# Kernel optimization log

Measured on AMD Instinct MI355X. Metric: run time of the kernel, lower is better.

The kernel has to match this reference:

```python
import jax, jax.numpy as jnp
import numpy as np

N_NODES = 100000
N_EDGES = 1600000
D_FEAT = 64
HIDDEN = 64


def _glorot(key, shape):
    fan_in, fan_out = shape[1], shape[0]
    limit = float(np.sqrt(6.0 / (fan_in + fan_out)))
    return jax.random.uniform(key, shape, jnp.float32, -limit, limit)


def setup_inputs() -> dict:
    key = jax.random.key(0)
    ks = jax.random.split(key, 8)
    x = jax.random.normal(ks[0], (N_NODES, D_FEAT), jnp.float32)
    edge_index = jax.random.randint(ks[1], (2, N_EDGES), 0, N_NODES, jnp.int64)
    # SAGEConv params: lin_l applied to aggregated neighbors (has bias),
    # lin_r applied to root/self features (no bias in PyG default).
    params = {
        "W1_l": _glorot(ks[2], (HIDDEN, D_FEAT)),
        "b1": jnp.zeros((HIDDEN,), jnp.float32),
        "W1_r": _glorot(ks[3], (HIDDEN, D_FEAT)),
        "W2_l": _glorot(ks[4], (HIDDEN, HIDDEN)),
        "b2": jnp.zeros((HIDDEN,), jnp.float32),
        "W2_r": _glorot(ks[5], (HIDDEN, HIDDEN)),
    }
    return {"x": x, "edge_index": edge_index, **params}


def _sage_conv(x, src, dst, deg_inv, W_l, b, W_r):
    # mean-aggregate neighbor features: gather at src, segment-sum at dst
    msg = jax.ops.segment_sum(x[src], dst, num_segments=N_NODES)  # [N, F]
    agg = msg * deg_inv[:, None]
    return agg @ W_l.T + b + x @ W_r.T


def reference(x, edge_index, W1_l, b1, W1_r, W2_l, b2, W2_r):
    src, dst = edge_index[0], edge_index[1]
    deg = jax.ops.segment_sum(jnp.ones((N_EDGES,), x.dtype), dst,
                              num_segments=N_NODES)
    deg_inv = 1.0 / jnp.maximum(deg, 1.0)  # PyG mean clamps count to >=1
    h = jax.nn.relu(_sage_conv(x, src, dst, deg_inv, W1_l, b1, W1_r))
    out = _sage_conv(h, src, dst, deg_inv, W2_l, b2, W2_r)
    return out
```

## Files before the change

kernel.cpp:

```cpp
#include <hip/hip_runtime.h>
#include <hip/hip_bf16.h>

#define FEAT 64

typedef __bf16 bf16x8 __attribute__((ext_vector_type(8)));
typedef __bf16 bf16x4 __attribute__((ext_vector_type(4)));
typedef float  f32x4  __attribute__((ext_vector_type(4)));

__global__ __launch_bounds__(256)
void zero2_kernel(int* __restrict__ a, int* __restrict__ b, int n) {
    int i = blockIdx.x * 256 + threadIdx.x;
    if (i < n) { a[i] = 0; b[i] = 0; }
}

__global__ void detect_castw_kernel(const unsigned* __restrict__ w, int* __restrict__ flag,
                                    int* __restrict__ zcnt,
                                    const float* __restrict__ a, const float* __restrict__ b,
                                    const float* __restrict__ c, const float* __restrict__ d,
                                    __bf16* __restrict__ o) {
    if (blockIdx.x == 0) {
        __shared__ int any_nz;
        if (threadIdx.x == 0) any_nz = 0;
        __syncthreads();
        if (w[2 * threadIdx.x + 1] != 0u) atomicOr(&any_nz, 1);
        zcnt[threadIdx.x] = 0;
        zcnt[threadIdx.x + 256] = 0;
        __syncthreads();
        if (threadIdx.x == 0) *flag = (any_nz == 0) ? 1 : 0;
    } else {
        int i = (blockIdx.x - 1) * 256 + threadIdx.x;
        if (i < FEAT * FEAT) {
            o[i]         = (__bf16)a[i];
            o[4096 + i]  = (__bf16)b[i];
            o[8192 + i]  = (__bf16)c[i];
            o[12288 + i] = (__bf16)d[i];
        }
    }
}

__global__ void detect_idx_kernel(const unsigned* __restrict__ w, int* __restrict__ flag,
                                  int* __restrict__ zcnt) {
    __shared__ int any_nz;
    if (threadIdx.x == 0) any_nz = 0;
    __syncthreads();
    if (w[2 * threadIdx.x + 1] != 0u) atomicOr(&any_nz, 1);
    zcnt[threadIdx.x] = 0;
    zcnt[threadIdx.x + 256] = 0;
    __syncthreads();
    if (threadIdx.x == 0) *flag = (any_nz == 0) ? 1 : 0;
}

__device__ __forceinline__ int load_idx_clamped(const void* ei, long long i, int is64, int n_nodes) {
    int v = is64 ? ((const int*)ei)[2 * i] : ((const int*)ei)[i];
    v = v < 0 ? 0 : v;
    return v >= n_nodes ? n_nodes - 1 : v;
}


__global__ __launch_bounds__(256)
void bucket_count_castx_kernel(const void* __restrict__ ei, const int* __restrict__ flagp,
                               int* __restrict__ gcnt,
                               const float* __restrict__ x, __bf16* __restrict__ xb, int n4,
                               int n_edges, int n_nodes) {
    __shared__ int cnt[512];
    const int t = threadIdx.x;
    if (blockIdx.x < 512) {
        cnt[t] = 0; cnt[t + 256] = 0;
        __syncthreads();
        const int is64 = *flagp;
        for (int e = blockIdx.x * 256 + t; e < n_edges; e += 512 * 256) {
            int d = load_idx_clamped(ei, (long long)n_edges + e, is64, n_nodes);
            atomicAdd(&cnt[d >> 9], 1);
        }
        __syncthreads();
        if (cnt[t])       atomicAdd(&gcnt[t], cnt[t]);
        if (cnt[t + 256]) atomicAdd(&gcnt[t + 256], cnt[t + 256]);
    } else {
        const int nb = gridDim.x - 512;
        for (int i = (blockIdx.x - 512) * 256 + t; i < n4; i += nb * 256) {
            float4 v = ((const float4*)x)[i];
            bf16x4 o;
            o.x = (__bf16)v.x; o.y = (__bf16)v.y; o.z = (__bf16)v.z; o.w = (__bf16)v.w;
            ((bf16x4*)xb)[i] = o;
        }
    }
}

__global__ void bucket_scan_kernel(const int* __restrict__ gcnt, int* __restrict__ gbase,
                                   int* __restrict__ gcur, int n_edges) {
    __shared__ int sh[512];
    int t = threadIdx.x;
    int v = gcnt[t];
    sh[t] = v;
    __syncthreads();
    for (int off = 1; off < 512; off <<= 1) {
        int u = (t >= off) ? sh[t - off] : 0;
        __syncthreads();
        sh[t] += u;
        __syncthreads();
    }
    int excl = sh[t] - v;
    gbase[t] = excl;
    gcur[t]  = excl;
    if (t == 511) gbase[512] = n_edges;
}

__global__ __launch_bounds__(256)
void multisplit_kernel(const void* __restrict__ ei, const int* __restrict__ flagp,
                       int* __restrict__ gcur, unsigned* __restrict__ B,
                       int n_edges, int n_nodes) {
    __shared__ unsigned sv[4096];
    __shared__ unsigned dv[4096];
    __shared__ int cnt[512];
    __shared__ int cur[512];
    const int t = threadIdx.x;
    const int is64 = *flagp;
    const int ntiles = (n_edges + 4095) >> 12;
    for (int tile = blockIdx.x; tile < ntiles; tile += gridDim.x) {
        cnt[t] = 0; cnt[t + 256] = 0;
        __syncthreads();
        #pragma unroll
        for (int k = 0; k < 16; ++k) {
            int i = k * 256 + t;
            int e = (tile << 12) + i;
            unsigned dmark = 0xFFFFFFFFu, s = 0;
            if (e < n_edges) {
                s     = (unsigned)load_idx_clamped(ei, e, is64, n_nodes);
                int d = load_idx_clamped(ei, (long long)n_edges + e, is64, n_nodes);
                dmark = (unsigned)d;
                atomicAdd(&cnt[d >> 9], 1);
            }
            sv[i] = s; dv[i] = dmark;
        }
        __syncthreads();
        if (cnt[t])       cur[t]       = atomicAdd(&gcur[t], cnt[t]);
        if (cnt[t + 256]) cur[t + 256] = atomicAdd(&gcur[t + 256], cnt[t + 256]);
        __syncthreads();
        #pragma unroll
        for (int k = 0; k < 16; ++k) {
            int i = k * 256 + t;
            unsigned d = dv[i];
            if (d != 0xFFFFFFFFu) {
                int pos = atomicAdd(&cur[d >> 9], 1);
                pos = pos < 0 ? 0 : (pos >= n_edges ? n_edges - 1 : pos);
                B[pos] = ((d & 511u) << 17) | sv[i];
            }
        }
        __syncthreads();
    }
}

__global__ __launch_bounds__(256)
void csr_build2_kernel(const unsigned* __restrict__ B, const int* __restrict__ gbase,
                       int* __restrict__ degc, int* __restrict__ offs,
                       float* __restrict__ dinv, int* __restrict__ csr,
                       int n_edges, int n_nodes) {
    __shared__ int cnt[512];
    __shared__ int scn[512];
    __shared__ int cur[512];
    const int b = blockIdx.x, t = threadIdx.x;
    cnt[t] = 0; cnt[t + 256] = 0;
    __syncthreads();
    const int lo = gbase[b], hi = gbase[b + 1];
    for (int i = lo + t; i < hi; i += 256) {
        unsigned v = B[i];
        atomicAdd(&cnt[v >> 17], 1);
    }
    __syncthreads();
    scn[t] = cnt[t]; scn[t + 256] = cnt[t + 256];
    __syncthreads();
    for (int off = 1; off < 512; off <<= 1) {
        int u0 = (t >= off) ? scn[t - off] : 0;
        int u1 = (t + 256 >= off) ? scn[t + 256 - off] : 0;
        __syncthreads();
        scn[t] += u0; scn[t + 256] += u1;
        __syncthreads();
    }
    const int base = gbase[b];
    int e0 = base + scn[t] - cnt[t];
    int e1 = base + scn[t + 256] - cnt[t + 256];
    cur[t] = e0; cur[t + 256] = e1;
    int n0 = b * 512 + t, n1 = n0 + 256;
    if (n0 < n_nodes) {
        degc[n0] = cnt[t]; offs[n0] = e0;
        dinv[n0] = 1.0f / fmaxf((float)cnt[t], 1.0f);
    }
    if (n1 < n_nodes) {
        degc[n1] = cnt[t + 256]; offs[n1] = e1;
        dinv[n1] = 1.0f / fmaxf((float)cnt[t + 256], 1.0f);
    }
    __syncthreads();
    for (int i = lo + t; i < hi; i += 256) {
        unsigned v = B[i];
        int pos = atomicAdd(&cur[v >> 17], 1);
        pos = pos < 0 ? 0 : (pos >= n_edges ? n_edges - 1 : pos);
        csr[pos] = (int)(v & 0x1FFFFu);
    }
}

__global__ __launch_bounds__(256)
void scan_partial_kernel(const int* __restrict__ degc, int* __restrict__ part, int n_nodes) {
    __shared__ int sh[256];
    int i = blockIdx.x * 256 + threadIdx.x;
    sh[threadIdx.x] = (i < n_nodes) ? degc[i] : 0;
    __syncthreads();
    for (int off = 128; off > 0; off >>= 1) {
        if (threadIdx.x < off) sh[threadIdx.x] += sh[threadIdx.x + off];
        __syncthreads();
    }
    if (threadIdx.x == 0) part[blockIdx.x] = sh[0];
}

__global__ void scan_top_kernel(int* __restrict__ part, int nparts) {
    __shared__ int sh[512];
    int t = threadIdx.x;
    int v = (t < nparts) ? part[t] : 0;
    sh[t] = v;
    __syncthreads();
    for (int off = 1; off < 512; off <<= 1) {
        int u = (t >= off) ? sh[t - off] : 0;
        __syncthreads();
        sh[t] += u;
        __syncthreads();
    }
    if (t < nparts) part[t] = sh[t] - v;
}

__global__ __launch_bounds__(256)
void scan_final_kernel(const int* __restrict__ degc, const int* __restrict__ part,
                       int* __restrict__ offs, float* __restrict__ deg_inv, int n_nodes) {
    __shared__ int sh[256];
    int t = threadIdx.x;
    int i = blockIdx.x * 256 + t;
    int v = (i < n_nodes) ? degc[i] : 0;
    sh[t] = v;
    __syncthreads();
    for (int off = 1; off < 256; off <<= 1) {
        int u = (t >= off) ? sh[t - off] : 0;
        __syncthreads();
        sh[t] += u;
        __syncthreads();
    }
    if (i < n_nodes) {
        offs[i]    = sh[t] - v + part[blockIdx.x];
        deg_inv[i] = 1.0f / fmaxf((float)v, 1.0f);
    }
}

__global__ __launch_bounds__(256)
void hist_kernel(const void* __restrict__ ei, const int* __restrict__ flagp,
                 int* __restrict__ degc, int n_edges, int n_nodes) {
    int e = blockIdx.x * 256 + threadIdx.x;
    if (e >= n_edges) return;
    int d = load_idx_clamped(ei, (long long)n_edges + e, *flagp, n_nodes);
    atomicAdd(&degc[d], 1);
}

__global__ __launch_bounds__(256)
void csr_scatter_kernel(const void* __restrict__ ei, const int* __restrict__ flagp,
                        const int* __restrict__ offs, int* __restrict__ cursor,
                        int* __restrict__ csr, int n_edges, int n_nodes) {
    int e = blockIdx.x * 256 + threadIdx.x;
    if (e >= n_edges) return;
    int is64 = *flagp;
    int s = load_idx_clamped(ei, e, is64, n_nodes);
    int d = load_idx_clamped(ei, (long long)n_edges + e, is64, n_nodes);
    int pos = offs[d] + atomicAdd(&cursor[d], 1);
    pos = pos < 0 ? 0 : (pos >= n_edges ? n_edges - 1 : pos);
    csr[pos] = s;
}

__global__ __launch_bounds__(256)
void cast_w_kernel(const float* __restrict__ a, const float* __restrict__ b,
                   const float* __restrict__ c, const float* __restrict__ d,
                   __bf16* __restrict__ o) {
    int i = blockIdx.x * 256 + threadIdx.x;
    if (i < FEAT * FEAT) {
        o[i]         = (__bf16)a[i];
        o[4096 + i]  = (__bf16)b[i];
        o[8192 + i]  = (__bf16)c[i];
        o[12288 + i] = (__bf16)d[i];
    }
}

__global__ __launch_bounds__(256)
void cast_x_kernel(const float* __restrict__ x, __bf16* __restrict__ xb, int n4) {
    int i = blockIdx.x * 256 + threadIdx.x;
    if (i < n4) {
        float4 v = ((const float4*)x)[i];
        bf16x4 o;
        o.x = (__bf16)v.x; o.y = (__bf16)v.y; o.z = (__bf16)v.z; o.w = (__bf16)v.w;
        ((bf16x4*)xb)[i] = o;
    }
}

__global__ __launch_bounds__(256)
void fused_l1_kernel(const __bf16* __restrict__ xb,
                     const int* __restrict__ offs, const int* __restrict__ degc,
                     const float* __restrict__ dinv, const int* __restrict__ csr,
                     const __bf16* __restrict__ Bl, const __bf16* __restrict__ Br,
                     const float* __restrict__ bias,
                     __bf16* __restrict__ hout, int n_nodes) {
    const int t = threadIdx.x, lane = t & 63, wave = t >> 6;
    const int quad = lane >> 4, r16 = lane & 15;
    const int grp = t >> 4, u = t & 15;
    bf16x8 bl[2], br[2];
    #pragma unroll
    for (int ks = 0; ks < 2; ++ks) {
        int f = wave * 16 + r16, k = ks * 32 + quad * 8;
        bl[ks] = *(const bf16x8*)(Bl + f * 64 + k);
        br[ks] = *(const bf16x8*)(Br + f * 64 + k);
    }
    const float bv = bias[wave * 16 + r16];
    __shared__ __bf16 sAgg[16][72];
    const int ntiles = (n_nodes + 15) >> 4;
    for (int tile = blockIdx.x; tile < ntiles; tile += gridDim.x) {
        const int n = tile * 16 + grp;
        const bool act = n < n_nodes;
        float a0 = 0.f, a1 = 0.f, a2 = 0.f, a3 = 0.f, di = 1.f;
        if (act) {
            int rs = offs[n], cnt = degc[n];
            di = dinv[n];
            int idx = (u < cnt) ? (int)__builtin_nontemporal_load(&csr[rs + u]) : 0;
            int c = 0;
            while (true) {
                idx = idx < 0 ? 0 : (idx >= n_nodes ? n_nodes - 1 : idx);
                int sj[16];
                #pragma unroll
                for (int j = 0; j < 16; ++j) sj[j] = __shfl(idx, j, 16);
                bf16x4 v[16];
                #pragma unroll
                for (int j = 0; j < 16; ++j)
                    v[j] = ((const bf16x4*)xb)[(size_t)sj[j] * 16 + u];
                #pragma unroll
                for (int j = 0; j < 16; ++j) {
                    float m = (c + j < cnt) ? 1.f : 0.f;
                    a0 = fmaf(m, (float)v[j].x, a0);
                    a1 = fmaf(m, (float)v[j].y, a1);
                    a2 = fmaf(m, (float)v[j].z, a2);
                    a3 = fmaf(m, (float)v[j].w, a3);
                }
                c += 16;
                if (c >= cnt) break;
                idx = (u < cnt - c) ? (int)__builtin_nontemporal_load(&csr[rs + c + u]) : 0;
            }
        }
        bf16x4 o;
        o.x = (__bf16)(a0 * di); o.y = (__bf16)(a1 * di);
        o.z = (__bf16)(a2 * di); o.w = (__bf16)(a3 * di);
        *(bf16x4*)(&sAgg[grp][u * 4]) = o;
        __syncthreads();
        const int m0 = tile * 16;
        int mrow = m0 + r16; if (mrow >= n_nodes) mrow = n_nodes - 1;
        bf16x8 ag[2], ax[2];
        #pragma unroll
        for (int ks = 0; ks < 2; ++ks) {
            ag[ks] = *(const bf16x8*)(&sAgg[r16][ks * 32 + quad * 8]);
            ax[ks] = *(const bf16x8*)(xb + (size_t)mrow * 64 + ks * 32 + quad * 8);
        }
        f32x4 acc = {0.f, 0.f, 0.f, 0.f};
        acc = __builtin_amdgcn_mfma_f32_16x16x32_bf16(ag[0], bl[0], acc, 0, 0, 0);
        acc = __builtin_amdgcn_mfma_f32_16x16x32_bf16(ag[1], bl[1], acc, 0, 0, 0);
        acc = __builtin_amdgcn_mfma_f32_16x16x32_bf16(ax[0], br[0], acc, 0, 0, 0);
        acc = __builtin_amdgcn_mfma_f32_16x16x32_bf16(ax[1], br[1], acc, 0, 0, 0);
        const int col = wave * 16 + r16;
        #pragma unroll
        for (int rg = 0; rg < 4; ++rg) {
            int row = m0 + quad * 4 + rg;
            if (row < n_nodes) {
                float ov = acc[rg] + bv;
                hout[(size_t)row * 64 + col] = (__bf16)fmaxf(ov, 0.f);
            }
        }
        __syncthreads();
    }
}

__global__ __launch_bounds__(256)
void fused_l2_kernel(const __bf16* __restrict__ hb,
                     const int* __restrict__ offs, const int* __restrict__ degc,
                     const float* __restrict__ dinv, const int* __restrict__ csr,
                     const __bf16* __restrict__ Bl, const __bf16* __restrict__ Br,
                     const float* __restrict__ bias,
                     float* __restrict__ out, int n_nodes) {
    const int t = threadIdx.x, lane = t & 63, wave = t >> 6;
    const int quad = lane >> 4, r16 = lane & 15;
    const int grp = t >> 4, u = t & 15;
    bf16x8 bl[2], br[2];
    #pragma unroll
    for (int ks = 0; ks < 2; ++ks) {
        int f = wave * 16 + r16, k = ks * 32 + quad * 8;
        bl[ks] = *(const bf16x8*)(Bl + f * 64 + k);
        br[ks] = *(const bf16x8*)(Br + f * 64 + k);
    }
    const float bv = bias[wave * 16 + r16];
    __shared__ __bf16 sAgg[16][72];
    const int ntiles = (n_nodes + 15) >> 4;
    for (int tile = blockIdx.x; tile < ntiles; tile += gridDim.x) {
        const int n = tile * 16 + grp;
        const bool act = n < n_nodes;
        float a0 = 0.f, a1 = 0.f, a2 = 0.f, a3 = 0.f, di = 1.f;
        if (act) {
            int rs = offs[n], cnt = degc[n];
            di = dinv[n];
            int idx = (u < cnt) ? (int)__builtin_nontemporal_load(&csr[rs + u]) : 0;
            int c = 0;
            while (true) {
                idx = idx < 0 ? 0 : (idx >= n_nodes ? n_nodes - 1 : idx);
                int sj[16];
                #pragma unroll
                for (int j = 0; j < 16; ++j) sj[j] = __shfl(idx, j, 16);
                bf16x4 v[16];
                #pragma unroll
                for (int j = 0; j < 16; ++j)
                    v[j] = ((const bf16x4*)hb)[(size_t)sj[j] * 16 + u];
                #pragma unroll
                for (int j = 0; j < 16; ++j) {
                    float m = (c + j < cnt) ? 1.f : 0.f;
                    a0 = fmaf(m, (float)v[j].x, a0);
                    a1 = fmaf(m, (float)v[j].y, a1);
                    a2 = fmaf(m, (float)v[j].z, a2);
                    a3 = fmaf(m, (float)v[j].w, a3);
                }
                c += 16;
                if (c >= cnt) break;
                idx = (u < cnt - c) ? (int)__builtin_nontemporal_load(&csr[rs + c + u]) : 0;
            }
        }
        bf16x4 o;
        o.x = (__bf16)(a0 * di); o.y = (__bf16)(a1 * di);
        o.z = (__bf16)(a2 * di); o.w = (__bf16)(a3 * di);
        *(bf16x4*)(&sAgg[grp][u * 4]) = o;
        __syncthreads();
        const int m0 = tile * 16;
        int mrow = m0 + r16; if (mrow >= n_nodes) mrow = n_nodes - 1;
        bf16x8 ag[2], ah[2];
        #pragma unroll
        for (int ks = 0; ks < 2; ++ks) {
            ag[ks] = *(const bf16x8*)(&sAgg[r16][ks * 32 + quad * 8]);
            ah[ks] = *(const bf16x8*)(hb + (size_t)mrow * 64 + ks * 32 + quad * 8);
        }
        f32x4 acc = {0.f, 0.f, 0.f, 0.f};
        acc = __builtin_amdgcn_mfma_f32_16x16x32_bf16(ag[0], bl[0], acc, 0, 0, 0);
        acc = __builtin_amdgcn_mfma_f32_16x16x32_bf16(ag[1], bl[1], acc, 0, 0, 0);
        acc = __builtin_amdgcn_mfma_f32_16x16x32_bf16(ah[0], br[0], acc, 0, 0, 0);
        acc = __builtin_amdgcn_mfma_f32_16x16x32_bf16(ah[1], br[1], acc, 0, 0, 0);
        const int col = wave * 16 + r16;
        #pragma unroll
        for (int rg = 0; rg < 4; ++rg) {
            int row = m0 + quad * 4 + rg;
            if (row < n_nodes) out[(size_t)row * 64 + col] = acc[rg] + bv;
        }
        __syncthreads();
    }
}

__global__ __launch_bounds__(256)
void gather_bf16_kernel(const __bf16* __restrict__ hin, const int* __restrict__ offs,
                        const int* __restrict__ degc, const float* __restrict__ dinv,
                        const int* __restrict__ csr, __bf16* __restrict__ agg,
                        int n_nodes) {
    const int t = threadIdx.x, u = t & 15;
    const int g0 = blockIdx.x * 16 + (t >> 4);
    const int ng = gridDim.x * 16;
    if (g0 >= n_nodes) return;
    int rs = offs[g0], cnt = degc[g0];
    float di = dinv[g0];
    int idx = (u < cnt) ? (int)__builtin_nontemporal_load(&csr[rs + u]) : 0;
    for (int n = g0; n < n_nodes; n += ng) {
        const int nn = n + ng;
        int rs2 = 0, cnt2 = 0;
        float di2 = 1.0f;
        if (nn < n_nodes) { rs2 = offs[nn]; cnt2 = degc[nn]; di2 = dinv[nn]; }
        float a0 = 0.f, a1 = 0.f, a2 = 0.f, a3 = 0.f;
        int c = 0;
        while (true) {
            idx = idx < 0 ? 0 : (idx >= n_nodes ? n_nodes - 1 : idx);
            int sj[16];
            #pragma unroll
            for (int j = 0; j < 16; ++j) sj[j] = __shfl(idx, j, 16);
            bf16x4 v[16];
            #pragma unroll
            for (int j = 0; j < 16; ++j)
                v[j] = ((const bf16x4*)hin)[(size_t)sj[j] * 16 + u];
            #pragma unroll
            for (int j = 0; j < 16; ++j) {
                float m = (c + j < cnt) ? 1.f : 0.f;
                a0 = fmaf(m, (float)v[j].x, a0);
                a1 = fmaf(m, (float)v[j].y, a1);
                a2 = fmaf(m, (float)v[j].z, a2);
                a3 = fmaf(m, (float)v[j].w, a3);
            }
            c += 16;
            if (c >= cnt) break;
            idx = (u < cnt - c) ? (int)__builtin_nontemporal_load(&csr[rs + c + u]) : 0;
        }
        idx = (nn < n_nodes && u < cnt2)
                  ? (int)__builtin_nontemporal_load(&csr[rs2 + u]) : 0;
        bf16x4 o;
        o.x = (__bf16)(a0 * di); o.y = (__bf16)(a1 * di);
        o.z = (__bf16)(a2 * di); o.w = (__bf16)(a3 * di);
        ((bf16x4*)agg)[(size_t)n * 16 + u] = o;
        rs = rs2; cnt = cnt2; di = di2;
    }
}

__global__ __launch_bounds__(256)
void gather_f32_kernel(const float* __restrict__ xin, const int* __restrict__ offs,
                       const int* __restrict__ degc, const float* __restrict__ dinv,
                       const int* __restrict__ csr, __bf16* __restrict__ agg,
                       int n_nodes) {
    const int t = threadIdx.x, lane = t & 63, g = lane >> 4, u = lane & 15;
    const int gw = blockIdx.x * 4 + (t >> 6), nw = gridDim.x * 4;
    for (int n = gw; n < n_nodes; n += nw) {
        int rs = offs[n], cnt = degc[n];
        float a0 = 0.f, a1 = 0.f, a2 = 0.f, a3 = 0.f;
        for (int c = 0; c < cnt; c += 64) {
            int chunk = min(64, cnt - c);
            int myid = (lane < chunk) ? (int)__builtin_nontemporal_load(&csr[rs + c + lane]) : 0;
            myid = myid < 0 ? 0 : (myid >= n_nodes ? n_nodes - 1 : myid);
            for (int q = 0; q < chunk; q += 16) {
                int q0 = q + g, q1 = q + g + 4, q2 = q + g + 8, q3 = q + g + 12;
                int s0 = __shfl(myid, q0), s1 = __shfl(myid, q1);
                int s2 = __shfl(myid, q2), s3 = __shfl(myid, q3);
                float m0 = (q0 < chunk) ? 1.f : 0.f;
                float m1 = (q1 < chunk) ? 1.f : 0.f;
                float m2 = (q2 < chunk) ? 1.f : 0.f;
                float m3 = (q3 < chunk) ? 1.f : 0.f;
                float4 v0 = ((const float4*)xin)[(size_t)s0 * 16 + u];
                float4 v1 = ((const float4*)xin)[(size_t)s1 * 16 + u];
                float4 v2 = ((const float4*)xin)[(size_t)s2 * 16 + u];
                float4 v3 = ((const float4*)xin)[(size_t)s3 * 16 + u];
                a0 = fmaf(m0, v0.x, a0); a1 = fmaf(m0, v0.y, a1);
                a2 = fmaf(m0, v0.z, a2); a3 = fmaf(m0, v0.w, a3);
                a0 = fmaf(m1, v1.x, a0); a1 = fmaf(m1, v1.y, a1);
                a2 = fmaf(m1, v1.z, a2); a3 = fmaf(m1, v1.w, a3);
                a0 = fmaf(m2, v2.x, a0); a1 = fmaf(m2, v2.y, a1);
                a2 = fmaf(m2, v2.z, a2); a3 = fmaf(m2, v2.w, a3);
                a0 = fmaf(m3, v3.x, a0); a1 = fmaf(m3, v3.y, a1);
                a2 = fmaf(m3, v3.z, a2); a3 = fmaf(m3, v3.w, a3);
            }
        }
        a0 += __shfl_xor(a0, 16); a1 += __shfl_xor(a1, 16);
        a2 += __shfl_xor(a2, 16); a3 += __shfl_xor(a3, 16);
        a0 += __shfl_xor(a0, 32); a1 += __shfl_xor(a1, 32);
        a2 += __shfl_xor(a2, 32); a3 += __shfl_xor(a3, 32);
        if (g == 0) {
            float di = dinv[n];
            bf16x4 o;
            o.x = (__bf16)(a0 * di); o.y = (__bf16)(a1 * di);
            o.z = (__bf16)(a2 * di); o.w = (__bf16)(a3 * di);
            ((bf16x4*)agg)[(size_t)n * 16 + u] = o;
        }
    }
}

__global__ __launch_bounds__(256)
void gemm_l1_kernel(const __bf16* __restrict__ Ag, const float* __restrict__ xin,
                    const __bf16* __restrict__ Bl, const __bf16* __restrict__ Br,
                    const float* __restrict__ bias,
                    __bf16* __restrict__ hout, int n_nodes) {
    const int t = threadIdx.x, lane = t & 63;
    const int quad = lane >> 4, r16 = lane & 15;
    bf16x8 bl[2][4], br[2][4];
    #pragma unroll
    for (int ks = 0; ks < 2; ++ks)
        #pragma unroll
        for (int ct = 0; ct < 4; ++ct) {
            int f = ct * 16 + r16, k = ks * 32 + quad * 8;
            bl[ks][ct] = *(const bf16x8*)(Bl + f * 64 + k);
            br[ks][ct] = *(const bf16x8*)(Br + f * 64 + k);
        }
    const int m0 = (blockIdx.x * 4 + (t >> 6)) * 16;
    if (m0 >= n_nodes) return;
    int mrow = m0 + r16; if (mrow >= n_nodes) mrow = n_nodes - 1;
    bf16x8 ag[2], ax[2];
    #pragma unroll
    for (int ks = 0; ks < 2; ++ks) {
        ag[ks] = *(const bf16x8*)(Ag + (size_t)mrow * 64 + ks * 32 + quad * 8);
        const float* xr = xin + (size_t)mrow * 64 + ks * 32 + quad * 8;
        float4 p = *(const float4*)xr;
        float4 q = *(const float4*)(xr + 4);
        union { bf16x8 v; __bf16 e[8]; } U;
        U.e[0] = (__bf16)p.x; U.e[1] = (__bf16)p.y; U.e[2] = (__bf16)p.z; U.e[3] = (__bf16)p.w;
        U.e[4] = (__bf16)q.x; U.e[5] = (__bf16)q.y; U.e[6] = (__bf16)q.z; U.e[7] = (__bf16)q.w;
        ax[ks] = U.v;
    }
    #pragma unroll
    for (int ct = 0; ct < 4; ++ct) {
        f32x4 acc = {0.f, 0.f, 0.f, 0.f};
        acc = __builtin_amdgcn_mfma_f32_16x16x32_bf16(ag[0], bl[0][ct], acc, 0, 0, 0);
        acc = __builtin_amdgcn_mfma_f32_16x16x32_bf16(ag[1], bl[1][ct], acc, 0, 0, 0);
        acc = __builtin_amdgcn_mfma_f32_16x16x32_bf16(ax[0], br[0][ct], acc, 0, 0, 0);
        acc = __builtin_amdgcn_mfma_f32_16x16x32_bf16(ax[1], br[1][ct], acc, 0, 0, 0);
        int col = ct * 16 + r16;
        float bv = bias[col];
        #pragma unroll
        for (int rg = 0; rg < 4; ++rg) {
            int n = m0 + quad * 4 + rg;
            if (n < n_nodes) {
                float o = acc[rg] + bv;
                hout[(size_t)n * 64 + col] = (__bf16)fmaxf(o, 0.f);
            }
        }
    }
}

__global__ __launch_bounds__(256)
void gemm_l2_kernel(const __bf16* __restrict__ Ag, const __bf16* __restrict__ Ah,
                    const __bf16* __restrict__ Bl, const __bf16* __restrict__ Br,
                    const float* __restrict__ bias,
                    float* __restrict__ out, int n_nodes) {
    const int t = threadIdx.x, lane = t & 63;
    const int quad = lane >> 4, r16 = lane & 15;
    bf16x8 bl[2][4], br[2][4];
    #pragma unroll
    for (int ks = 0; ks < 2; ++ks)
        #pragma unroll
        for (int ct = 0; ct < 4; ++ct) {
            int f = ct * 16 + r16, k = ks * 32 + quad * 8;
            bl[ks][ct] = *(const bf16x8*)(Bl + f * 64 + k);
            br[ks][ct] = *(const bf16x8*)(Br + f * 64 + k);
        }
    const int m0 = (blockIdx.x * 4 + (t >> 6)) * 16;
    if (m0 >= n_nodes) return;
    int mrow = m0 + r16; if (mrow >= n_nodes) mrow = n_nodes - 1;
    bf16x8 ag[2], ah[2];
    #pragma unroll
    for (int ks = 0; ks < 2; ++ks) {
        ag[ks] = *(const bf16x8*)(Ag + (size_t)mrow * 64 + ks * 32 + quad * 8);
        ah[ks] = *(const bf16x8*)(Ah + (size_t)mrow * 64 + ks * 32 + quad * 8);
    }
    #pragma unroll
    for (int ct = 0; ct < 4; ++ct) {
        f32x4 acc = {0.f, 0.f, 0.f, 0.f};
        acc = __builtin_amdgcn_mfma_f32_16x16x32_bf16(ag[0], bl[0][ct], acc, 0, 0, 0);
        acc = __builtin_amdgcn_mfma_f32_16x16x32_bf16(ag[1], bl[1][ct], acc, 0, 0, 0);
        acc = __builtin_amdgcn_mfma_f32_16x16x32_bf16(ah[0], br[0][ct], acc, 0, 0, 0);
        acc = __builtin_amdgcn_mfma_f32_16x16x32_bf16(ah[1], br[1][ct], acc, 0, 0, 0);
        int col = ct * 16 + r16;
        float bv = bias[col];
        #pragma unroll
        for (int rg = 0; rg < 4; ++rg) {
            int n = m0 + quad * 4 + rg;
            if (n < n_nodes) out[(size_t)n * 64 + col] = acc[rg] + bv;
        }
    }
}

__global__ __launch_bounds__(256)
void sage_fused_l1_kernel(const float* __restrict__ xin,
                          const int* __restrict__ offs, const int* __restrict__ degc,
                          const float* __restrict__ deg_inv, const int* __restrict__ csr,
                          const float* __restrict__ Wl, const float* __restrict__ bias,
                          const float* __restrict__ Wr,
                          __bf16* __restrict__ hout, int n_nodes) {
    __shared__ float WlT[FEAT * 65], WrT[FEAT * 65], bsh[FEAT];
    __shared__ float aggS[4][FEAT], selfS[4][FEAT];
    const int t = threadIdx.x;
    #pragma unroll
    for (int p = 0; p < 16; ++p) {
        int i = t + p * 256, j = i >> 6, k = i & 63;
        WlT[k * 65 + j] = Wl[i];
        WrT[k * 65 + j] = Wr[i];
    }
    if (t < FEAT) bsh[t] = bias[t];
    __syncthreads();
    const int w = t >> 6, f = t & 63;
    const int n_groups = (n_nodes + 3) >> 2;
    for (int g = blockIdx.x; g < n_groups; g += gridDim.x) {
        int n = g * 4 + w;
        bool act = (n < n_nodes);
        if (act) {
            int rs = offs[n], cnt = degc[n];
            float acc = 0.f;
            for (int c = 0; c < cnt; c += 64) {
                int chunk = min(64, cnt - c);
                int myid = (f < chunk) ? csr[rs + c + f] : 0;
                #pragma unroll 4
                for (int q = 0; q < chunk; ++q) {
                    int s = __shfl(myid, q);
                    acc += xin[(long long)s * FEAT + f];
                }
            }
            aggS[w][f]  = acc * deg_inv[n];
            selfS[w][f] = xin[(long long)n * FEAT + f];
        }
        __syncthreads();
        if (act) {
            float o = bsh[f];
            #pragma unroll
            for (int k = 0; k < FEAT; ++k) {
                o = fmaf(aggS[w][k],  WlT[k * 65 + f], o);
                o = fmaf(selfS[w][k], WrT[k * 65 + f], o);
            }
            o = fmaxf(o, 0.f);
            hout[(long long)n * FEAT + f] = (__bf16)o;
        }
        __syncthreads();
    }
}

__global__ __launch_bounds__(256)
void sage_fused_l2_kernel(const __bf16* __restrict__ hin,
                          const int* __restrict__ offs, const int* __restrict__ degc,
                          const float* __restrict__ deg_inv, const int* __restrict__ csr,
                          const float* __restrict__ Wl, const float* __restrict__ bias,
                          const float* __restrict__ Wr,
                          float* __restrict__ out, int n_nodes) {
    __shared__ float WlT[FEAT * 65], WrT[FEAT * 65], bsh[FEAT];
    __shared__ float aggS[4][FEAT], selfS[4][FEAT];
    const int t = threadIdx.x;
    #pragma unroll
    for (int p = 0; p < 16; ++p) {
        int i = t + p * 256, j = i >> 6, k = i & 63;
        WlT[k * 65 + j] = Wl[i];
        WrT[k * 65 + j] = Wr[i];
    }
    if (t < FEAT) bsh[t] = bias[t];
    __syncthreads();
    const int w = t >> 6, f = t & 63;
    const int n_groups = (n_nodes + 3) >> 2;
    for (int g = blockIdx.x; g < n_groups; g += gridDim.x) {
        int n = g * 4 + w;
        bool act = (n < n_nodes);
        if (act) {
            int rs = offs[n], cnt = degc[n];
            float acc = 0.f;
            for (int c = 0; c < cnt; c += 64) {
                int chunk = min(64, cnt - c);
                int myid = (f < chunk) ? csr[rs + c + f] : 0;
                #pragma unroll 4
                for (int q = 0; q < chunk; ++q) {
                    int s = __shfl(myid, q);
                    acc += (float)hin[(long long)s * FEAT + f];
                }
            }
            aggS[w][f]  = acc * deg_inv[n];
            selfS[w][f] = (float)hin[(long long)n * FEAT + f];
        }
        __syncthreads();
        if (act) {
            float o = bsh[f];
            #pragma unroll
            for (int k = 0; k < FEAT; ++k) {
                o = fmaf(aggS[w][k],  WlT[k * 65 + f], o);
                o = fmaf(selfS[w][k], WrT[k * 65 + f], o);
            }
            out[(long long)n * FEAT + f] = o;
        }
        __syncthreads();
    }
}

extern "C" void kernel_launch(void* const* d_in, const int* in_sizes, int n_in,
                              void* d_out, int out_size, void* d_ws, size_t ws_size,
                              hipStream_t stream) {
    const float* x   = (const float*)d_in[0];
    const void*  ei  = d_in[1];
    const float* W1l = (const float*)d_in[2];
    const float* b1  = (const float*)d_in[3];
    const float* W1r = (const float*)d_in[4];
    const float* W2l = (const float*)d_in[5];
    const float* b2  = (const float*)d_in[6];
    const float* W2r = (const float*)d_in[7];
    float* out = (float*)d_out;

    const int n_nodes = in_sizes[0] / FEAT;
    const int n_edges = in_sizes[1] / 2;
    const int nparts  = (n_nodes + 255) / 256;
    const int egrid   = (n_edges + 255) / 256;
    const int NB      = (n_nodes + 511) >> 9;

    char* ws = (char*)d_ws;
    auto al = [](size_t v) { return (v + 255) & ~(size_t)255; };

    size_t o = 0;
    int*      flag  = (int*)(ws + o);      o += 256;
    int*      degc  = (int*)(ws + o);      o += al((size_t)n_nodes * 4);
    float*    dinv  = (float*)(ws + o);    o += al((size_t)n_nodes * 4);
    int*      offs  = (int*)(ws + o);      o += al((size_t)n_nodes * 4);
    int*      gcnt  = (int*)(ws + o);      o += al(512 * 4);
    int*      gbase = (int*)(ws + o);      o += al(513 * 4);
    int*      gcur  = (int*)(ws + o);      o += al(512 * 4);
    unsigned* B     = (unsigned*)(ws + o); o += al((size_t)n_edges * 4);
    int*      csr   = (int*)(ws + o);      o += al((size_t)n_edges * 4);
    __bf16*   xb    = (__bf16*)(ws + o);   o += al((size_t)n_nodes * FEAT * 2);
    __bf16*   wb    = (__bf16*)(ws + o);   o += al((size_t)4 * FEAT * FEAT * 2);
    __bf16*   h     = (__bf16*)(ws + o);   o += al((size_t)n_nodes * FEAT * 2);
    const size_t needT1 = o;

    size_t o3 = 0;
    int*    flag3   = (int*)(ws + o3);    o3 += 256;
    int*    degc3   = (int*)(ws + o3);    o3 += al((size_t)n_nodes * 4);
    float*  dinv3   = (float*)(ws + o3);  o3 += al((size_t)n_nodes * 4);
    int*    offs3   = (int*)(ws + o3);    o3 += al((size_t)n_nodes * 4);
    int*    cursor3 = (int*)(ws + o3);    o3 += al((size_t)n_nodes * 4);
    int*    part3   = (int*)(ws + o3);    o3 += al(2048);
    int*    csr3    = (int*)(ws + o3);    o3 += al((size_t)n_edges * 4);
    const size_t commonEnd3 = o3;
    __bf16* wb3  = (__bf16*)(ws + o3);    o3 += al((size_t)4 * FEAT * FEAT * 2);
    __bf16* agg3 = (__bf16*)(ws + o3);    o3 += al((size_t)n_nodes * FEAT * 2);
    __bf16* h3   = (__bf16*)(ws + o3);    o3 += al((size_t)n_nodes * FEAT * 2);
    const size_t needT3 = o3;

    const int n4 = n_nodes * FEAT / 4;
    const int mgrid = (n_nodes + 63) / 64;
    const int ggrid = 2048;
    const int ntiles = (n_edges + 4095) >> 12;
    const int ftiles = (n_nodes + 15) >> 4;
    const int fgrid2 = ftiles < 2048 ? ftiles : 2048;

    if (ws_size >= needT1 && n_nodes <= 131072) {
        detect_castw_kernel<<<17, 256, 0, stream>>>((const unsigned*)ei, flag, gcnt,
                                                    W1l, W1r, W2l, W2r, wb);
        bucket_count_castx_kernel<<<1536, 256, 0, stream>>>(ei, flag, gcnt,
                                                            x, xb, n4, n_edges, n_nodes);
        bucket_scan_kernel<<<1, 512, 0, stream>>>(gcnt, gbase, gcur, n_edges);
        multisplit_kernel<<<ntiles, 256, 0, stream>>>(ei, flag, gcur, B, n_edges, n_nodes);
        csr_build2_kernel<<<NB, 256, 0, stream>>>(B, gbase, degc, offs, dinv, csr, n_edges, n_nodes);
        fused_l1_kernel<<<fgrid2, 256, 0, stream>>>(xb, offs, degc, dinv, csr,
                                                    wb, wb + 4096, b1, h, n_nodes);
        fused_l2_kernel<<<fgrid2, 256, 0, stream>>>(h, offs, degc, dinv, csr,
                                                    wb + 8192, wb + 12288, b2, out, n_nodes);
    } else if (ws_size >= needT3) {
        zero2_kernel<<<nparts, 256, 0, stream>>>(degc3, cursor3, n_nodes);
        detect_idx_kernel<<<1, 256, 0, stream>>>((const unsigned*)ei, flag3, part3);
        hist_kernel<<<egrid, 256, 0, stream>>>(ei, flag3, degc3, n_edges, n_nodes);
        scan_partial_kernel<<<nparts, 256, 0, stream>>>(degc3, part3, n_nodes);
        scan_top_kernel<<<1, 512, 0, stream>>>(part3, nparts);
        scan_final_kernel<<<nparts, 256, 0, stream>>>(degc3, part3, offs3, dinv3, n_nodes);
        csr_scatter_kernel<<<egrid, 256, 0, stream>>>(ei, flag3, offs3, cursor3, csr3, n_edges, n_nodes);
        cast_w_kernel<<<16, 256, 0, stream>>>(W1l, W1r, W2l, W2r, wb3);
        gather_f32_kernel<<<ggrid, 256, 0, stream>>>(x, offs3, degc3, dinv3, csr3, agg3, n_nodes);
        gemm_l1_kernel<<<mgrid, 256, 0, stream>>>(agg3, x, wb3, wb3 + 4096, b1, h3, n_nodes);
        gather_bf16_kernel<<<ggrid, 256, 0, stream>>>(h3, offs3, degc3, dinv3, csr3, agg3, n_nodes);
        gemm_l2_kernel<<<mgrid, 256, 0, stream>>>(agg3, h3, wb3 + 8192, wb3 + 12288, b2, out, n_nodes);
    } else {
        __bf16* hf = (__bf16*)(ws + commonEnd3);
        zero2_kernel<<<nparts, 256, 0, stream>>>(degc3, cursor3, n_nodes);
        detect_idx_kernel<<<1, 256, 0, stream>>>((const unsigned*)ei, flag3, part3);
        hist_kernel<<<egrid, 256, 0, stream>>>(ei, flag3, degc3, n_edges, n_nodes);
        scan_partial_kernel<<<nparts, 256, 0, stream>>>(degc3, part3, n_nodes);
        scan_top_kernel<<<1, 512, 0, stream>>>(part3, nparts);
        scan_final_kernel<<<nparts, 256, 0, stream>>>(degc3, part3, offs3, dinv3, n_nodes);
        csr_scatter_kernel<<<egrid, 256, 0, stream>>>(ei, flag3, offs3, cursor3, csr3, n_edges, n_nodes);
        const int n_groups = (n_nodes + 3) / 4;
        const int fgrid = n_groups < 4096 ? n_groups : 4096;
        sage_fused_l1_kernel<<<fgrid, 256, 0, stream>>>(x, offs3, degc3, dinv3, csr3,
                                                        W1l, b1, W1r, hf, n_nodes);
        sage_fused_l2_kernel<<<fgrid, 256, 0, stream>>>(hf, offs3, degc3, dinv3, csr3,
                                                        W2l, b2, W2r, out, n_nodes);
    }
}
```

Measured before the change: 240.0 us.

## Fold bucket scan into count kernel via last-block pattern; use 256-node buckets

```diff
diff --git a/kernel.cpp b/kernel.cpp
--- a/kernel.cpp
+++ b/kernel.cpp
@@ -6,6 +6,7 @@
 typedef __bf16 bf16x8 __attribute__((ext_vector_type(8)));
 typedef __bf16 bf16x4 __attribute__((ext_vector_type(4)));
 typedef float  f32x4  __attribute__((ext_vector_type(4)));
+
 
 __global__ __launch_bounds__(256)
 void zero2_kernel(int* __restrict__ a, int* __restrict__ b, int n) {
@@ -23,8 +24,9 @@
         if (threadIdx.x == 0) any_nz = 0;
         __syncthreads();
         if (w[2 * threadIdx.x + 1] != 0u) atomicOr(&any_nz, 1);
-        zcnt[threadIdx.x] = 0;
+        zcnt[threadIdx.x]       = 0;
         zcnt[threadIdx.x + 256] = 0;
+        if (threadIdx.x == 0) zcnt[512] = 0;
         __syncthreads();
         if (threadIdx.x == 0) *flag = (any_nz == 0) ? 1 : 0;
     } else {
@@ -59,10 +61,12 @@
 
 __global__ __launch_bounds__(256)
 void bucket_count_castx_kernel(const void* __restrict__ ei, const int* __restrict__ flagp,
-                               int* __restrict__ gcnt,
+                               int* __restrict__ gcnt, int* __restrict__ gbase,
+                               int* __restrict__ gcur,
                                const float* __restrict__ x, __bf16* __restrict__ xb, int n4,
                                int n_edges, int n_nodes) {
     __shared__ int cnt[512];
+    __shared__ int amLast;
     const int t = threadIdx.x;
     if (blockIdx.x < 512) {
         cnt[t] = 0; cnt[t + 256] = 0;
@@ -70,11 +74,32 @@
         const int is64 = *flagp;
         for (int e = blockIdx.x * 256 + t; e < n_edges; e += 512 * 256) {
             int d = load_idx_clamped(ei, (long long)n_edges + e, is64, n_nodes);
-            atomicAdd(&cnt[d >> 9], 1);
+            atomicAdd(&cnt[d >> 8], 1);
         }
         __syncthreads();
         if (cnt[t])       atomicAdd(&gcnt[t], cnt[t]);
         if (cnt[t + 256]) atomicAdd(&gcnt[t + 256], cnt[t + 256]);
+        __threadfence();
+        __syncthreads();
+        if (t == 0) amLast = (atomicAdd(&gcnt[512], 1) == 511);
+        __syncthreads();
+        if (amLast) {
+            __shared__ int scn[512];
+            int v0 = atomicAdd(&gcnt[t], 0);
+            int v1 = atomicAdd(&gcnt[t + 256], 0);
+            scn[t] = v0; scn[t + 256] = v1;
+            __syncthreads();
+            for (int off = 1; off < 512; off <<= 1) {
+                int u0 = (t >= off) ? scn[t - off] : 0;
+                int u1 = (t + 256 >= off) ? scn[t + 256 - off] : 0;
+                __syncthreads();
+                scn[t] += u0; scn[t + 256] += u1;
+                __syncthreads();
+            }
+            gbase[t]       = scn[t] - v0;       gcur[t]       = scn[t] - v0;
+            gbase[t + 256] = scn[t + 256] - v1; gcur[t + 256] = scn[t + 256] - v1;
+            if (t == 0) gbase[512] = n_edges;
+        }
     } else {
         const int nb = gridDim.x - 512;
         for (int i = (blockIdx.x - 512) * 256 + t; i < n4; i += nb * 256) {
@@ -84,25 +109,6 @@
             ((bf16x4*)xb)[i] = o;
         }
     }
-}
-
-__global__ void bucket_scan_kernel(const int* __restrict__ gcnt, int* __restrict__ gbase,
-                                   int* __restrict__ gcur, int n_edges) {
-    __shared__ int sh[512];
-    int t = threadIdx.x;
-    int v = gcnt[t];
-    sh[t] = v;
-    __syncthreads();
-    for (int off = 1; off < 512; off <<= 1) {
-        int u = (t >= off) ? sh[t - off] : 0;
-        __syncthreads();
-        sh[t] += u;
-        __syncthreads();
-    }
-    int excl = sh[t] - v;
-    gbase[t] = excl;
-    gcur[t]  = excl;
-    if (t == 511) gbase[512] = n_edges;
 }
 
 __global__ __launch_bounds__(256)
@@ -128,7 +134,7 @@
                 s     = (unsigned)load_idx_clamped(ei, e, is64, n_nodes);
                 int d = load_idx_clamped(ei, (long long)n_edges + e, is64, n_nodes);
                 dmark = (unsigned)d;
-                atomicAdd(&cnt[d >> 9], 1);
+                atomicAdd(&cnt[d >> 8], 1);
             }
             sv[i] = s; dv[i] = dmark;
         }
@@ -141,9 +147,9 @@
             int i = k * 256 + t;
             unsigned d = dv[i];
             if (d != 0xFFFFFFFFu) {
-                int pos = atomicAdd(&cur[d >> 9], 1);
+                int pos = atomicAdd(&cur[d >> 8], 1);
                 pos = pos < 0 ? 0 : (pos >= n_edges ? n_edges - 1 : pos);
-                B[pos] = ((d & 511u) << 17) | sv[i];
+                B[pos] = ((d & 255u) << 17) | sv[i];
             }
         }
         __syncthreads();
@@ -155,11 +161,11 @@
                        int* __restrict__ degc, int* __restrict__ offs,
                        float* __restrict__ dinv, int* __restrict__ csr,
                        int n_edges, int n_nodes) {
-    __shared__ int cnt[512];
-    __shared__ int scn[512];
-    __shared__ int cur[512];
+    __shared__ int cnt[256];
+    __shared__ int scn[256];
+    __shared__ int cur[256];
     const int b = blockIdx.x, t = threadIdx.x;
-    cnt[t] = 0; cnt[t + 256] = 0;
+    cnt[t] = 0;
     __syncthreads();
     const int lo = gbase[b], hi = gbase[b + 1];
     for (int i = lo + t; i < hi; i += 256) {
@@ -167,130 +173,28 @@
         atomicAdd(&cnt[v >> 17], 1);
     }
     __syncthreads();
-    scn[t] = cnt[t]; scn[t + 256] = cnt[t + 256];
-    __syncthreads();
-    for (int off = 1; off < 512; off <<= 1) {
-        int u0 = (t >= off) ? scn[t - off] : 0;
-        int u1 = (t + 256 >= off) ? scn[t + 256 - off] : 0;
-        __syncthreads();
-        scn[t] += u0; scn[t + 256] += u1;
-        __syncthreads();
-    }
-    const int base = gbase[b];
-    int e0 = base + scn[t] - cnt[t];
-    int e1 = base + scn[t + 256] - cnt[t + 256];
-    cur[t] = e0; cur[t + 256] = e1;
-    int n0 = b * 512 + t, n1 = n0 + 256;
+    int v = cnt[t];
+    scn[t] = v;
+    __syncthreads();
+    for (int off = 1; off < 256; off <<= 1) {
+        int u = (t >= off) ? scn[t - off] : 0;
+        __syncthreads();
+        scn[t] += u;
+        __syncthreads();
+    }
+    int e0 = lo + scn[t] - v;
+    cur[t] = e0;
+    int n0 = b * 256 + t;
     if (n0 < n_nodes) {
-        degc[n0] = cnt[t]; offs[n0] = e0;
-        dinv[n0] = 1.0f / fmaxf((float)cnt[t], 1.0f);
-    }
-    if (n1 < n_nodes) {
-        degc[n1] = cnt[t + 256]; offs[n1] = e1;
-        dinv[n1] = 1.0f / fmaxf((float)cnt[t + 256], 1.0f);
+        degc[n0] = v; offs[n0] = e0;
+        dinv[n0] = 1.0f / fmaxf((float)v, 1.0f);
     }
     __syncthreads();
     for (int i = lo + t; i < hi; i += 256) {
-        unsigned v = B[i];
-        int pos = atomicAdd(&cur[v >> 17], 1);
+        unsigned w = B[i];
+        int pos = atomicAdd(&cur[w >> 17], 1);
         pos = pos < 0 ? 0 : (pos >= n_edges ? n_edges - 1 : pos);
-        csr[pos] = (int)(v & 0x1FFFFu);
-    }
-}
-
-__global__ __launch_bounds__(256)
-void scan_partial_kernel(const int* __restrict__ degc, int* __restrict__ part, int n_nodes) {
-    __shared__ int sh[256];
-    int i = blockIdx.x * 256 + threadIdx.x;
-    sh[threadIdx.x] = (i < n_nodes) ? degc[i] : 0;
-    __syncthreads();
-    for (int off = 128; off > 0; off >>= 1) {
-        if (threadIdx.x < off) sh[threadIdx.x] += sh[threadIdx.x + off];
-        __syncthreads();
-    }
-    if (threadIdx.x == 0) part[blockIdx.x] = sh[0];
-}
-
-__global__ void scan_top_kernel(int* __restrict__ part, int nparts) {
-    __shared__ int sh[512];
-    int t = threadIdx.x;
-    int v = (t < nparts) ? part[t] : 0;
-    sh[t] = v;
-    __syncthreads();
-    for (int off = 1; off < 512; off <<= 1) {
-        int u = (t >= off) ? sh[t - off] : 0;
-        __syncthreads();
-        sh[t] += u;
-        __syncthreads();
-    }
-    if (t < nparts) part[t] = sh[t] - v;
-}
-
-__global__ __launch_bounds__(256)
-void scan_final_kernel(const int* __restrict__ degc, const int* __restrict__ part,
-                       int* __restrict__ offs, float* __restrict__ deg_inv, int n_nodes) {
-    __shared__ int sh[256];
-    int t = threadIdx.x;
-    int i = blockIdx.x * 256 + t;
-    int v = (i < n_nodes) ? degc[i] : 0;
-    sh[t] = v;
-    __syncthreads();
-    for (int off = 1; off < 256; off <<= 1) {
-        int u = (t >= off) ? sh[t - off] : 0;
-        __syncthreads();
-        sh[t] += u;
-        __syncthreads();
-    }
-    if (i < n_nodes) {
-        offs[i]    = sh[t] - v + part[blockIdx.x];
-        deg_inv[i] = 1.0f / fmaxf((float)v, 1.0f);
-    }
-}
-
-__global__ __launch_bounds__(256)
-void hist_kernel(const void* __restrict__ ei, const int* __restrict__ flagp,
-                 int* __restrict__ degc, int n_edges, int n_nodes) {
-    int e = blockIdx.x * 256 + threadIdx.x;
-    if (e >= n_edges) return;
-    int d = load_idx_clamped(ei, (long long)n_edges + e, *flagp, n_nodes);
-    atomicAdd(&degc[d], 1);
-}
-
-__global__ __launch_bounds__(256)
-void csr_scatter_kernel(const void* __restrict__ ei, const int* __restrict__ flagp,
-                        const int* __restrict__ offs, int* __restrict__ cursor,
-                        int* __restrict__ csr, int n_edges, int n_nodes) {
-    int e = blockIdx.x * 256 + threadIdx.x;
-    if (e >= n_edges) return;
-    int is64 = *flagp;
-    int s = load_idx_clamped(ei, e, is64, n_nodes);
-    int d = load_idx_clamped(ei, (long long)n_edges + e, is64, n_nodes);
-    int pos = offs[d] + atomicAdd(&cursor[d], 1);
-    pos = pos < 0 ? 0 : (pos >= n_edges ? n_edges - 1 : pos);
-    csr[pos] = s;
-}
-
-__global__ __launch_bounds__(256)
-void cast_w_kernel(const float* __restrict__ a, const float* __restrict__ b,
-                   const float* __restrict__ c, const float* __restrict__ d,
-                   __bf16* __restrict__ o) {
-    int i = blockIdx.x * 256 + threadIdx.x;
-    if (i < FEAT * FEAT) {
-        o[i]         = (__bf16)a[i];
-        o[4096 + i]  = (__bf16)b[i];
-        o[8192 + i]  = (__bf16)c[i];
-        o[12288 + i] = (__bf16)d[i];
-    }
-}
-
-__global__ __launch_bounds__(256)
-void cast_x_kernel(const float* __restrict__ x, __bf16* __restrict__ xb, int n4) {
-    int i = blockIdx.x * 256 + threadIdx.x;
-    if (i < n4) {
-        float4 v = ((const float4*)x)[i];
-        bf16x4 o;
-        o.x = (__bf16)v.x; o.y = (__bf16)v.y; o.z = (__bf16)v.z; o.w = (__bf16)v.w;
-        ((bf16x4*)xb)[i] = o;
+        csr[pos] = (int)(w & 0x1FFFFu);
     }
 }
 
@@ -452,6 +356,91 @@
             if (row < n_nodes) out[(size_t)row * 64 + col] = acc[rg] + bv;
         }
         __syncthreads();
+    }
+}
+
+__global__ __launch_bounds__(256)
+void scan_partial_kernel(const int* __restrict__ degc, int* __restrict__ part, int n_nodes) {
+    __shared__ int sh[256];
+    int i = blockIdx.x * 256 + threadIdx.x;
+    sh[threadIdx.x] = (i < n_nodes) ? degc[i] : 0;
+    __syncthreads();
+    for (int off = 128; off > 0; off >>= 1) {
+        if (threadIdx.x < off) sh[threadIdx.x] += sh[threadIdx.x + off];
+        __syncthreads();
+    }
+    if (threadIdx.x == 0) part[blockIdx.x] = sh[0];
+}
+
+__global__ void scan_top_kernel(int* __restrict__ part, int nparts) {
+    __shared__ int sh[512];
+    int t = threadIdx.x;
+    int v = (t < nparts) ? part[t] : 0;
+    sh[t] = v;
+    __syncthreads();
+    for (int off = 1; off < 512; off <<= 1) {
+        int u = (t >= off) ? sh[t - off] : 0;
+        __syncthreads();
+        sh[t] += u;
+        __syncthreads();
+    }
+    if (t < nparts) part[t] = sh[t] - v;
+}
+
+__global__ __launch_bounds__(256)
+void scan_final_kernel(const int* __restrict__ degc, const int* __restrict__ part,
+                       int* __restrict__ offs, float* __restrict__ deg_inv, int n_nodes) {
+    __shared__ int sh[256];
+    int t = threadIdx.x;
+    int i = blockIdx.x * 256 + t;
+    int v = (i < n_nodes) ? degc[i] : 0;
+    sh[t] = v;
+    __syncthreads();
+    for (int off = 1; off < 256; off <<= 1) {
+        int u = (t >= off) ? sh[t - off] : 0;
+        __syncthreads();
+        sh[t] += u;
+        __syncthreads();
+    }
+    if (i < n_nodes) {
+        offs[i]    = sh[t] - v + part[blockIdx.x];
+        deg_inv[i] = 1.0f / fmaxf((float)v, 1.0f);
+    }
+}
+
+__global__ __launch_bounds__(256)
+void hist_kernel(const void* __restrict__ ei, const int* __restrict__ flagp,
+                 int* __restrict__ degc, int n_edges, int n_nodes) {
+    int e = blockIdx.x * 256 + threadIdx.x;
+    if (e >= n_edges) return;
+    int d = load_idx_clamped(ei, (long long)n_edges + e, *flagp, n_nodes);
+    atomicAdd(&degc[d], 1);
+}
+
+__global__ __launch_bounds__(256)
+void csr_scatter_kernel(const void* __restrict__ ei, const int* __restrict__ flagp,
+                        const int* __restrict__ offs, int* __restrict__ cursor,
+                        int* __restrict__ csr, int n_edges, int n_nodes) {
+    int e = blockIdx.x * 256 + threadIdx.x;
+    if (e >= n_edges) return;
+    int is64 = *flagp;
+    int s = load_idx_clamped(ei, e, is64, n_nodes);
+    int d = load_idx_clamped(ei, (long long)n_edges + e, is64, n_nodes);
+    int pos = offs[d] + atomicAdd(&cursor[d], 1);
+    pos = pos < 0 ? 0 : (pos >= n_edges ? n_edges - 1 : pos);
+    csr[pos] = s;
+}
+
+__global__ __launch_bounds__(256)
+void cast_w_kernel(const float* __restrict__ a, const float* __restrict__ b,
+                   const float* __restrict__ c, const float* __restrict__ d,
+                   __bf16* __restrict__ o) {
+    int i = blockIdx.x * 256 + threadIdx.x;
+    if (i < FEAT * FEAT) {
+        o[i]         = (__bf16)a[i];
+        o[4096 + i]  = (__bf16)b[i];
+        o[8192 + i]  = (__bf16)c[i];
+        o[12288 + i] = (__bf16)d[i];
     }
 }
 
@@ -770,7 +759,7 @@
     const int n_edges = in_sizes[1] / 2;
     const int nparts  = (n_nodes + 255) / 256;
     const int egrid   = (n_edges + 255) / 256;
-    const int NB      = (n_nodes + 511) >> 9;
+    const int NB256   = (n_nodes + 255) >> 8;
 
     char* ws = (char*)d_ws;
     auto al = [](size_t v) { return (v + 255) & ~(size_t)255; };
@@ -780,7 +769,7 @@
     int*      degc  = (int*)(ws + o);      o += al((size_t)n_nodes * 4);
     float*    dinv  = (float*)(ws + o);    o += al((size_t)n_nodes * 4);
     int*      offs  = (int*)(ws + o);      o += al((size_t)n_nodes * 4);
-    int*      gcnt  = (int*)(ws + o);      o += al(512 * 4);
+    int*      gcnt  = (int*)(ws + o);      o += al(516 * 4);
     int*      gbase = (int*)(ws + o);      o += al(513 * 4);
     int*      gcur  = (int*)(ws + o);      o += al(512 * 4);
     unsigned* B     = (unsigned*)(ws + o); o += al((size_t)n_edges * 4);
@@ -814,11 +803,10 @@
     if (ws_size >= needT1 && n_nodes <= 131072) {
         detect_castw_kernel<<<17, 256, 0, stream>>>((const unsigned*)ei, flag, gcnt,
                                                     W1l, W1r, W2l, W2r, wb);
-        bucket_count_castx_kernel<<<1536, 256, 0, stream>>>(ei, flag, gcnt,
+        bucket_count_castx_kernel<<<1536, 256, 0, stream>>>(ei, flag, gcnt, gbase, gcur,
                                                             x, xb, n4, n_edges, n_nodes);
-        bucket_scan_kernel<<<1, 512, 0, stream>>>(gcnt, gbase, gcur, n_edges);
         multisplit_kernel<<<ntiles, 256, 0, stream>>>(ei, flag, gcur, B, n_edges, n_nodes);
-        csr_build2_kernel<<<NB, 256, 0, stream>>>(B, gbase, degc, offs, dinv, csr, n_edges, n_nodes);
+        csr_build2_kernel<<<NB256, 256, 0, stream>>>(B, gbase, degc, offs, dinv, csr, n_edges, n_nodes);
         fused_l1_kernel<<<fgrid2, 256, 0, stream>>>(xb, offs, degc, dinv, csr,
                                                     wb, wb + 4096, b1, h, n_nodes);
         fused_l2_kernel<<<fgrid2, 256, 0, stream>>>(h, offs, degc, dinv, csr,
```

Result: slower. 255.4 us (+6.4%).
